# Kernel optimization log

Hardware: AMD Instinct MI355X
Metric: run time of the kernel (lower is better)

The kernel has to match this reference:

```python
import jax, jax.numpy as jnp
import numpy as np

N_NODES = 100000
N_EDGES = 1600000
DIM = 128
N_LAYERS = 3
N_GRAPHS = 128
OUT = 2


def setup_inputs() -> dict:
    key = jax.random.key(0)
    ks = jax.random.split(key, 8)
    x = jax.random.normal(ks[0], (N_NODES, DIM), dtype=jnp.float32)
    edge_index = jax.random.randint(ks[1], (2, N_EDGES), 0, N_NODES, dtype=jnp.int32)
    batch = jnp.sort(jax.random.randint(ks[2], (N_NODES,), 0, N_GRAPHS, dtype=jnp.int32))
    s = 1.0 / np.sqrt(DIM)
    conv_w = jax.random.normal(ks[3], (N_LAYERS, DIM, DIM), dtype=jnp.float32) * s
    conv_b = jnp.zeros((N_LAYERS, DIM), dtype=jnp.float32)
    lin1_w = jax.random.normal(ks[4], (DIM, DIM), dtype=jnp.float32) * s
    lin1_b = jnp.zeros((DIM,), dtype=jnp.float32)
    lin2_w = jax.random.normal(ks[5], (DIM, OUT), dtype=jnp.float32) * s
    lin2_b = jnp.zeros((OUT,), dtype=jnp.float32)
    return {"x": x, "edge_index": edge_index, "batch": batch,
            "conv_w": conv_w, "conv_b": conv_b,
            "lin1_w": lin1_w, "lin1_b": lin1_b,
            "lin2_w": lin2_w, "lin2_b": lin2_b}


def _gcn_conv(x, src, dst, norm, w, b, n_nodes):
    # linear transform first (in==out==DIM), then gather-scale-scatter
    h = x @ w                                    # [N, dim]
    msg = h[src] * norm[:, None]                 # [E+N, dim] gathered messages
    out = jax.ops.segment_sum(msg, dst, num_segments=n_nodes)
    return out + b


def reference(x, edge_index, batch, conv_w, conv_b, lin1_w, lin1_b, lin2_w, lin2_b):
    n = x.shape[0]
    loop = jnp.arange(n, dtype=edge_index.dtype)
    src = jnp.concatenate([edge_index[0], loop])  # PyG: add self-loops
    dst = jnp.concatenate([edge_index[1], loop])
    # symmetric normalization: deg computed on destination (col) with self-loops
    deg = jax.ops.segment_sum(jnp.ones_like(dst, dtype=x.dtype), dst, num_segments=n)
    deg_inv_sqrt = jnp.where(deg > 0, jax.lax.rsqrt(jnp.maximum(deg, 1.0)), 0.0)
    norm = deg_inv_sqrt[src] * deg_inv_sqrt[dst]

    h = x
    for i in range(conv_w.shape[0]):  # fixed small layer count
        h = jax.nn.relu(_gcn_conv(h, src, dst, norm, conv_w[i], conv_b[i], n))

    # global mean pool over graphs in the batch
    sums = jax.ops.segment_sum(h, batch, num_segments=N_GRAPHS)
    cnts = jax.ops.segment_sum(jnp.ones((n,), dtype=h.dtype), batch, num_segments=N_GRAPHS)
    g = sums / jnp.maximum(cnts, 1.0)[:, None]   # [G, dim]

    g = jax.nn.relu(g @ lin1_w + lin1_b)
    # dropout is inference-mode identity (training=False)
    logits = g @ lin2_w + lin2_b
    return jax.nn.log_softmax(logits, axis=-1)
```

## Files before the change

### kernel.cpp

```cpp
#include <hip/hip_runtime.h>
#include <hip/hip_fp16.h>
#include <math.h>

#define DIM 128
#define POOL_SPLIT 32
#define BINSH 10
#define EPB 8192
#define PAD 18432

typedef __attribute__((ext_vector_type(8))) _Float16 half8;
typedef __attribute__((ext_vector_type(4))) float f32x4;
typedef __attribute__((ext_vector_type(2))) float f32x2;


__global__ __launch_bounds__(1024) void bin_k(const int* __restrict__ src,
                                              const int* __restrict__ dst,
                                              int* __restrict__ bincur,
                                              unsigned int* __restrict__ tmp,
                                              int E, int NBIN) {
    __shared__ int cur[128];
    const int t = threadIdx.x;
    if (t < 128) cur[t] = 0;
    __syncthreads();
    const int e0 = blockIdx.x * EPB;
    const int e1 = min(e0 + EPB, E);
    for (int e = e0 + t; e < e1; e += 1024)
        atomicAdd(&cur[dst[e] >> BINSH], 1);
    __syncthreads();
    if (t < NBIN) {
        int h = cur[t];
        cur[t] = h ? atomicAdd(&bincur[t * 16], h) : 0;
    }
    __syncthreads();
    for (int e = e0 + t; e < e1; e += 1024) {
        int d = dst[e], s = src[e];
        int b = d >> BINSH;
        int pos = atomicAdd(&cur[b], 1);
        if (pos < PAD)
            tmp[(size_t)b * PAD + pos] =
                (unsigned int)((s << BINSH) | (d & ((1 << BINSH) - 1)));
    }
}

__global__ void binscan_k(const int* __restrict__ bincur, int* __restrict__ binbase,
                          int NBIN) {
    __shared__ int s[128];
    const int t = threadIdx.x;
    int v = (t < NBIN) ? bincur[t * 16] : 0;
    s[t] = v;
    __syncthreads();
    for (int off = 1; off < 128; off <<= 1) {
        int u = (t >= off) ? s[t - off] : 0;
        __syncthreads();
        s[t] += u;
        __syncthreads();
    }
    int excl = s[t] - v;
    if (t < NBIN) binbase[t] = excl;
    if (t == 127) binbase[NBIN] = s[127];
}

__global__ __launch_bounds__(1024) void rowcnt_k(const unsigned int* __restrict__ tmp,
                                                 const int* __restrict__ bincur,
                                                 const int* __restrict__ binbase,
                                                 int* __restrict__ rowptr,
                                                 float* __restrict__ dis,
                                                 int n, int NBIN) {
    __shared__ int cnt[1 << BINSH];
    const int b = blockIdx.x, t = threadIdx.x;
    cnt[t] = 0;
    __syncthreads();
    const int size = bincur[b * 16];
    const unsigned int* bt = tmp + (size_t)b * PAD;
    for (int e = t; e < size; e += 1024)
        atomicAdd(&cnt[bt[e] & ((1 << BINSH) - 1)], 1);
    __syncthreads();
    int v = cnt[t];
    __syncthreads();
    for (int off = 1; off < 1024; off <<= 1) {
        int u = (t >= off) ? cnt[t - off] : 0;
        __syncthreads();
        cnt[t] += u;
        __syncthreads();
    }
    int excl = cnt[t] - v;
    int node = (b << BINSH) + t;
    if (node < n) {
        rowptr[node] = binbase[b] + excl;
        dis[node] = rsqrtf((float)(v + 1));
    }
    if (b == NBIN - 1 && t == 0) rowptr[n] = binbase[NBIN];
}

__global__ __launch_bounds__(1024) void fill_k(const unsigned int* __restrict__ tmp,
                                               const int* __restrict__ bincur,
                                               const int* __restrict__ rowptr,
                                               const float* __restrict__ dis,
                                               int2* __restrict__ ew, int n) {
    __shared__ int lcur[1 << BINSH];
    __shared__ float ldis[1 << BINSH];
    const int b = blockIdx.x, t = threadIdx.x;
    const int base_node = b << BINSH;
    if (base_node + t < n) {
        lcur[t] = rowptr[base_node + t];
        ldis[t] = dis[base_node + t];
    }
    __syncthreads();
    const int size = bincur[b * 16];
    const unsigned int* bt = tmp + (size_t)b * PAD;
    for (int e = t; e < size; e += 1024) {
        unsigned int u = bt[e];
        int sidx = (int)(u >> BINSH);
        int loc = (int)(u & ((1 << BINSH) - 1));
        float w = dis[sidx] * ldis[loc];
        int q = atomicAdd(&lcur[loc], 1);
        ew[q] = make_int2(sidx, __float_as_int(w));
    }
}

__global__ void wpack_k(const float* __restrict__ conv_w, _Float16* __restrict__ bp) {
    int g = blockIdx.x * 256 + threadIdx.x;
    if (g >= 3 * 2048) return;
    int l = g >> 11;
    int rem = g & 2047;
    int c = rem >> 8;
    int f = (rem >> 6) & 3;
    int lane = rem & 63;
    const float* W = conv_w + l * DIM * DIM;
    int kbase = f * 32 + (lane >> 4) * 8;
    int col = c * 16 + (lane & 15);
    _Float16* d = bp + ((size_t)l * 2048 + (size_t)(c * 4 + f) * 64 + lane) * 8;
#pragma unroll
    for (int j = 0; j < 8; ++j)
        d[j] = (_Float16)W[(kbase + j) * DIM + col];
}

template <bool FP16IN>
__global__ __launch_bounds__(256) void gemm_k(const void* __restrict__ Ain,
                                              const _Float16* __restrict__ Bp,
                                              unsigned int* __restrict__ T32, int n) {
    const int t = threadIdx.x;
    const int lane = t & 63;
    const int wave = t >> 6;
    const int quad = lane >> 4;
    const int m    = lane & 15;
    const int row  = blockIdx.x * 64 + wave * 16 + m;
    const bool act = row < n;

    half8 a[4];
    if (act) {
        if (FP16IN) {
            const _Float16* A = (const _Float16*)Ain + (size_t)row * DIM;
#pragma unroll
            for (int f = 0; f < 4; ++f)
                a[f] = *(const half8*)(A + f * 32 + quad * 8);
        } else {
            const float* A = (const float*)Ain + (size_t)row * DIM;
#pragma unroll
            for (int f = 0; f < 4; ++f) {
                float4 v0 = *(const float4*)(A + f * 32 + quad * 8);
                float4 v1 = *(const float4*)(A + f * 32 + quad * 8 + 4);
                __half2 h01 = __floats2half2_rn(v0.x, v0.y);
                __half2 h23 = __floats2half2_rn(v0.z, v0.w);
                __half2 h45 = __floats2half2_rn(v1.x, v1.y);
                __half2 h67 = __floats2half2_rn(v1.z, v1.w);
                int4 pk;
                pk.x = *(int*)&h01; pk.y = *(int*)&h23;
                pk.z = *(int*)&h45; pk.w = *(int*)&h67;
                a[f] = *(half8*)&pk;
            }
        }
    } else {
#pragma unroll
        for (int f = 0; f < 4; ++f) a[f] = half8{};
    }

    const half8* B8 = (const half8*)Bp;
#pragma unroll
    for (int c = 0; c < 8; ++c) {
        f32x4 acc = {0.f, 0.f, 0.f, 0.f};
#pragma unroll
        for (int f = 0; f < 4; ++f) {
            half8 b = B8[(c * 4 + f) * 64 + lane];
            acc = __builtin_amdgcn_mfma_f32_16x16x32_f16(b, a[f], acc, 0, 0, 0);
        }
        if (act) {
            int r = 0;
            r = __builtin_amdgcn_cvt_pk_fp8_f32(acc[0], acc[1], r, 0);
            r = __builtin_amdgcn_cvt_pk_fp8_f32(acc[2], acc[3], r, 1);
            T32[(size_t)row * 32 + c * 4 + quad] = (unsigned int)r;
        }
    }
}

#define ACC_EDGE(qq, rr) { \
    float w = __int_as_float(qq.y); \
    f32x2 a0 = __builtin_amdgcn_cvt_pk_f32_fp8((int)rr.x, 0); \
    f32x2 a1 = __builtin_amdgcn_cvt_pk_f32_fp8((int)rr.x, 1); \
    f32x2 a2 = __builtin_amdgcn_cvt_pk_f32_fp8((int)rr.y, 0); \
    f32x2 a3 = __builtin_amdgcn_cvt_pk_f32_fp8((int)rr.y, 1); \
    acc[0] += w * a0[0]; acc[1] += w * a0[1]; \
    acc[2] += w * a1[0]; acc[3] += w * a1[1]; \
    acc[4] += w * a2[0]; acc[5] += w * a2[1]; \
    acc[6] += w * a3[0]; acc[7] += w * a3[1]; }

__global__ __launch_bounds__(256) void agg_k(const unsigned int* __restrict__ T32,
                                             const int* __restrict__ rowptr,
                                             const int2* __restrict__ ew,
                                             const float* __restrict__ dis,
                                             const float* __restrict__ bias,
                                             __half* __restrict__ O, int n) {
    const int lane = threadIdx.x & 63;
    const int qd   = lane >> 4;
    const int li   = lane & 15;
    const int v = blockIdx.x * 16 + (threadIdx.x >> 6) * 4 + qd;
    const bool act = v < n;

    const uint2* T2 = (const uint2*)T32;

    float dv = act ? dis[v] : 0.f;
    int e0 = act ? rowptr[v] : 0;
    int e1 = act ? rowptr[v + 1] : 0;

    float acc[8] = {0.f, 0.f, 0.f, 0.f, 0.f, 0.f, 0.f, 0.f};

    if (act) {
        uint2 rs = T2[(size_t)v * 16 + li];
        float w = dv * dv;
        f32x2 a0 = __builtin_amdgcn_cvt_pk_f32_fp8((int)rs.x, 0);
        f32x2 a1 = __builtin_amdgcn_cvt_pk_f32_fp8((int)rs.x, 1);
        f32x2 a2 = __builtin_amdgcn_cvt_pk_f32_fp8((int)rs.y, 0);
        f32x2 a3 = __builtin_amdgcn_cvt_pk_f32_fp8((int)rs.y, 1);
        acc[0] += w * a0[0]; acc[1] += w * a0[1];
        acc[2] += w * a1[0]; acc[3] += w * a1[1];
        acc[4] += w * a2[0]; acc[5] += w * a2[1];
        acc[6] += w * a3[0]; acc[7] += w * a3[1];
    }

    int e = e0;
    for (; e + 8 <= e1; e += 8) {
        int2 q0 = ew[e + 0], q1 = ew[e + 1], q2 = ew[e + 2], q3 = ew[e + 3];
        int2 q4 = ew[e + 4], q5 = ew[e + 5], q6 = ew[e + 6], q7 = ew[e + 7];
        uint2 r0 = T2[(size_t)q0.x * 16 + li];
        uint2 r1 = T2[(size_t)q1.x * 16 + li];
        uint2 r2 = T2[(size_t)q2.x * 16 + li];
        uint2 r3 = T2[(size_t)q3.x * 16 + li];
        uint2 r4 = T2[(size_t)q4.x * 16 + li];
        uint2 r5 = T2[(size_t)q5.x * 16 + li];
        uint2 r6 = T2[(size_t)q6.x * 16 + li];
        uint2 r7 = T2[(size_t)q7.x * 16 + li];
        ACC_EDGE(q0, r0); ACC_EDGE(q1, r1);
        ACC_EDGE(q2, r2); ACC_EDGE(q3, r3);
        ACC_EDGE(q4, r4); ACC_EDGE(q5, r5);
        ACC_EDGE(q6, r6); ACC_EDGE(q7, r7);
    }
    for (; e + 4 <= e1; e += 4) {
        int2 q0 = ew[e + 0], q1 = ew[e + 1], q2 = ew[e + 2], q3 = ew[e + 3];
        uint2 r0 = T2[(size_t)q0.x * 16 + li];
        uint2 r1 = T2[(size_t)q1.x * 16 + li];
        uint2 r2 = T2[(size_t)q2.x * 16 + li];
        uint2 r3 = T2[(size_t)q3.x * 16 + li];
        ACC_EDGE(q0, r0); ACC_EDGE(q1, r1);
        ACC_EDGE(q2, r2); ACC_EDGE(q3, r3);
    }
    for (; e + 2 <= e1; e += 2) {
        int2 q0 = ew[e + 0], q1 = ew[e + 1];
        uint2 r0 = T2[(size_t)q0.x * 16 + li];
        uint2 r1 = T2[(size_t)q1.x * 16 + li];
        ACC_EDGE(q0, r0); ACC_EDGE(q1, r1);
    }
    if (e < e1) {
        int2 q0 = ew[e];
        uint2 r0 = T2[(size_t)q0.x * 16 + li];
        ACC_EDGE(q0, r0);
    }

    if (act) {
        float4 b0 = ((const float4*)bias)[li * 2 + 0];
        float4 b1 = ((const float4*)bias)[li * 2 + 1];
        __half2 o0 = __floats2half2_rn(fmaxf(acc[0] + b0.x, 0.f), fmaxf(acc[1] + b0.y, 0.f));
        __half2 o1 = __floats2half2_rn(fmaxf(acc[2] + b0.z, 0.f), fmaxf(acc[3] + b0.w, 0.f));
        __half2 o2 = __floats2half2_rn(fmaxf(acc[4] + b1.x, 0.f), fmaxf(acc[5] + b1.y, 0.f));
        __half2 o3 = __floats2half2_rn(fmaxf(acc[6] + b1.z, 0.f), fmaxf(acc[7] + b1.w, 0.f));
        int4 o;
        o.x = *(int*)&o0; o.y = *(int*)&o1; o.z = *(int*)&o2; o.w = *(int*)&o3;
        *(int4*)(O + (size_t)v * DIM + li * 8) = o;
    }
}

__global__ __launch_bounds__(64) void pool_k(const __half* __restrict__ H,
                                             const int* __restrict__ batch,
                                             float* __restrict__ G, int n) {
    int g = blockIdx.x;
    int part = blockIdx.y;

    int lo = 0, hi = n;
    while (lo < hi) { int m = (lo + hi) >> 1; if (batch[m] < g) lo = m + 1; else hi = m; }
    int start = lo;
    lo = start; hi = n;
    while (lo < hi) { int m = (lo + hi) >> 1; if (batch[m] < g + 1) lo = m + 1; else hi = m; }
    int end = lo;
    int cnt = end - start;
    if (cnt <= 0) return;
    float inv = 1.0f / (float)cnt;

    int lane = threadIdx.x;
    const __half2* H2 = (const __half2*)H;
    float2 s = make_float2(0.f, 0.f);
    for (int v = start + part; v < end; v += POOL_SPLIT) {
        float2 h = __half22float2(H2[(size_t)v * 64 + lane]);
        s.x += h.x; s.y += h.y;
    }
    atomicAdd(&G[g * DIM + 2 * lane + 0], s.x * inv);
    atomicAdd(&G[g * DIM + 2 * lane + 1], s.y * inv);
}

__global__ __launch_bounds__(128) void head_k(const float* __restrict__ G,
                                              const float* __restrict__ l1w,
                                              const float* __restrict__ l1b,
                                              const float* __restrict__ l2w,
                                              const float* __restrict__ l2b,
                                              float* __restrict__ out) {
    int g = blockIdx.x;
    int j = threadIdx.x;
    __shared__ float gs[128];
    __shared__ float2 red[128];

    gs[j] = G[g * 128 + j];
    __syncthreads();

    float acc = l1b[j];
    for (int k = 0; k < 128; ++k) acc += gs[k] * l1w[k * 128 + j];
    float y = fmaxf(acc, 0.f);

    red[j] = make_float2(y * l2w[j * 2 + 0], y * l2w[j * 2 + 1]);
    __syncthreads();
    for (int s = 64; s > 0; s >>= 1) {
        if (j < s) {
            red[j].x += red[j + s].x;
            red[j].y += red[j + s].y;
        }
        __syncthreads();
    }
    if (j == 0) {
        float l0 = red[0].x + l2b[0];
        float l1 = red[0].y + l2b[1];
        float m = fmaxf(l0, l1);
        float lse = m + logf(expf(l0 - m) + expf(l1 - m));
        out[g * 2 + 0] = l0 - lse;
        out[g * 2 + 1] = l1 - lse;
    }
}

extern "C" void kernel_launch(void* const* d_in, const int* in_sizes, int n_in,
                              void* d_out, int out_size, void* d_ws, size_t ws_size,
                              hipStream_t stream) {
    const float* x       = (const float*)d_in[0];
    const int*   ei      = (const int*)d_in[1];
    const int*   batch   = (const int*)d_in[2];
    const float* conv_w  = (const float*)d_in[3];
    const float* conv_b  = (const float*)d_in[4];
    const float* lin1_w  = (const float*)d_in[5];
    const float* lin1_b  = (const float*)d_in[6];
    const float* lin2_w  = (const float*)d_in[7];
    const float* lin2_b  = (const float*)d_in[8];
    float* out = (float*)d_out;

    const int n = in_sizes[0] / DIM;
    const int E = in_sizes[1] / 2;
    const int n_graphs = 128;
    const int NBIN = (n + (1 << BINSH) - 1) >> BINSH;

    const int* src = ei;
    const int* dst = ei + E;

    char* p = (char*)d_ws;
    auto alloc = [&](size_t bytes) {
        char* r = p;
        p += (bytes + 255) & ~(size_t)255;
        return r;
    };
    __half*        bufH    = (__half*)alloc((size_t)n * DIM * 2);
    unsigned int*  bufT    = (unsigned int*)alloc((size_t)n * DIM);
    float*         dis     = (float*)alloc((size_t)n * 4);
    int*           rowptr  = (int*)alloc((size_t)(n + 1) * 4);
    int*           binbase = (int*)alloc(132 * 4);
    int*           bincur  = (int*)alloc((size_t)NBIN * 16 * 4);
    unsigned int*  tmp     = (unsigned int*)alloc((size_t)NBIN * PAD * 4);
    int2*          ew      = (int2*)alloc((size_t)E * 8);
    float*         gbuf    = (float*)alloc((size_t)n_graphs * DIM * 4);
    _Float16*      bp      = (_Float16*)alloc((size_t)3 * 2048 * 8 * 2);
    (void)ws_size;

    const int binBlocks = (E + EPB - 1) / EPB;

    hipMemsetAsync(bincur, 0, (size_t)NBIN * 16 * 4, stream);
    hipMemsetAsync(gbuf, 0, (size_t)n_graphs * DIM * 4, stream);
    wpack_k<<<24, 256, 0, stream>>>(conv_w, bp);
    bin_k<<<binBlocks, 1024, 0, stream>>>(src, dst, bincur, tmp, E, NBIN);
    binscan_k<<<1, 128, 0, stream>>>(bincur, binbase, NBIN);
    rowcnt_k<<<NBIN, 1024, 0, stream>>>(tmp, bincur, binbase, rowptr, dis, n, NBIN);
    fill_k<<<NBIN, 1024, 0, stream>>>(tmp, bincur, rowptr, dis, ew, n);

    const int gemmBlocks = (n + 63) / 64;
    const int aggBlocks = (n + 15) / 16;

    gemm_k<false><<<gemmBlocks, 256, 0, stream>>>((const void*)x, bp + 0 * 16384, bufT, n);
    agg_k<<<aggBlocks, 256, 0, stream>>>(bufT, rowptr, ew, dis, conv_b + 0 * DIM, bufH, n);
    gemm_k<true><<<gemmBlocks, 256, 0, stream>>>((const void*)bufH, bp + 1 * 16384, bufT, n);
    agg_k<<<aggBlocks, 256, 0, stream>>>(bufT, rowptr, ew, dis, conv_b + 1 * DIM, bufH, n);
    gemm_k<true><<<gemmBlocks, 256, 0, stream>>>((const void*)bufH, bp + 2 * 16384, bufT, n);
    agg_k<<<aggBlocks, 256, 0, stream>>>(bufT, rowptr, ew, dis, conv_b + 2 * DIM, bufH, n);

    dim3 pgrid(n_graphs, POOL_SPLIT);
    pool_k<<<pgrid, 64, 0, stream>>>(bufH, batch, gbuf, n);
    head_k<<<n_graphs, 128, 0, stream>>>(gbuf, lin1_w, lin1_b, lin2_w, lin2_b, out);
}
```

Measured before the change: 349.3 us.

## Fuse CSR build kernels, fold normalization into GEMM, merge pool and head

Merges the row-count, scan and fill kernels into one per-bin kernel that stages the bin in LDS and writes a padded CSR with per-node start/end pairs. Edges drop from (src, weight) pairs to bare indices. The source-side deg^-1/2 is now applied in the GEMM epilogue before FP8 packing, and the destination-side factor once at the end of aggregation. The memsets are folded into a prep kernel, and pool plus head become a single kernel with 128 blocks. This cuts launches and edge-list bandwidth, but pooling now runs on far fewer threads, and scaling before FP8 quantization changes rounding behaviour.

```diff
diff --git a/kernel.cpp b/kernel.cpp
--- a/kernel.cpp
+++ b/kernel.cpp
@@ -3,7 +3,6 @@
 #include <math.h>
 
 #define DIM 128
-#define POOL_SPLIT 32
 #define BINSH 10
 #define EPB 8192
 #define PAD 18432
@@ -12,114 +11,11 @@
 typedef __attribute__((ext_vector_type(4))) float f32x4;
 typedef __attribute__((ext_vector_type(2))) float f32x2;
 
-
-__global__ __launch_bounds__(1024) void bin_k(const int* __restrict__ src,
-                                              const int* __restrict__ dst,
-                                              int* __restrict__ bincur,
-                                              unsigned int* __restrict__ tmp,
-                                              int E, int NBIN) {
-    __shared__ int cur[128];
-    const int t = threadIdx.x;
-    if (t < 128) cur[t] = 0;
-    __syncthreads();
-    const int e0 = blockIdx.x * EPB;
-    const int e1 = min(e0 + EPB, E);
-    for (int e = e0 + t; e < e1; e += 1024)
-        atomicAdd(&cur[dst[e] >> BINSH], 1);
-    __syncthreads();
-    if (t < NBIN) {
-        int h = cur[t];
-        cur[t] = h ? atomicAdd(&bincur[t * 16], h) : 0;
-    }
-    __syncthreads();
-    for (int e = e0 + t; e < e1; e += 1024) {
-        int d = dst[e], s = src[e];
-        int b = d >> BINSH;
-        int pos = atomicAdd(&cur[b], 1);
-        if (pos < PAD)
-            tmp[(size_t)b * PAD + pos] =
-                (unsigned int)((s << BINSH) | (d & ((1 << BINSH) - 1)));
-    }
-}
-
-__global__ void binscan_k(const int* __restrict__ bincur, int* __restrict__ binbase,
-                          int NBIN) {
-    __shared__ int s[128];
-    const int t = threadIdx.x;
-    int v = (t < NBIN) ? bincur[t * 16] : 0;
-    s[t] = v;
-    __syncthreads();
-    for (int off = 1; off < 128; off <<= 1) {
-        int u = (t >= off) ? s[t - off] : 0;
-        __syncthreads();
-        s[t] += u;
-        __syncthreads();
-    }
-    int excl = s[t] - v;
-    if (t < NBIN) binbase[t] = excl;
-    if (t == 127) binbase[NBIN] = s[127];
-}
-
-__global__ __launch_bounds__(1024) void rowcnt_k(const unsigned int* __restrict__ tmp,
-                                                 const int* __restrict__ bincur,
-                                                 const int* __restrict__ binbase,
-                                                 int* __restrict__ rowptr,
-                                                 float* __restrict__ dis,
-                                                 int n, int NBIN) {
-    __shared__ int cnt[1 << BINSH];
-    const int b = blockIdx.x, t = threadIdx.x;
-    cnt[t] = 0;
-    __syncthreads();
-    const int size = bincur[b * 16];
-    const unsigned int* bt = tmp + (size_t)b * PAD;
-    for (int e = t; e < size; e += 1024)
-        atomicAdd(&cnt[bt[e] & ((1 << BINSH) - 1)], 1);
-    __syncthreads();
-    int v = cnt[t];
-    __syncthreads();
-    for (int off = 1; off < 1024; off <<= 1) {
-        int u = (t >= off) ? cnt[t - off] : 0;
-        __syncthreads();
-        cnt[t] += u;
-        __syncthreads();
-    }
-    int excl = cnt[t] - v;
-    int node = (b << BINSH) + t;
-    if (node < n) {
-        rowptr[node] = binbase[b] + excl;
-        dis[node] = rsqrtf((float)(v + 1));
-    }
-    if (b == NBIN - 1 && t == 0) rowptr[n] = binbase[NBIN];
-}
-
-__global__ __launch_bounds__(1024) void fill_k(const unsigned int* __restrict__ tmp,
-                                               const int* __restrict__ bincur,
-                                               const int* __restrict__ rowptr,
-                                               const float* __restrict__ dis,
-                                               int2* __restrict__ ew, int n) {
-    __shared__ int lcur[1 << BINSH];
-    __shared__ float ldis[1 << BINSH];
-    const int b = blockIdx.x, t = threadIdx.x;
-    const int base_node = b << BINSH;
-    if (base_node + t < n) {
-        lcur[t] = rowptr[base_node + t];
-        ldis[t] = dis[base_node + t];
-    }
-    __syncthreads();
-    const int size = bincur[b * 16];
-    const unsigned int* bt = tmp + (size_t)b * PAD;
-    for (int e = t; e < size; e += 1024) {
-        unsigned int u = bt[e];
-        int sidx = (int)(u >> BINSH);
-        int loc = (int)(u & ((1 << BINSH) - 1));
-        float w = dis[sidx] * ldis[loc];
-        int q = atomicAdd(&lcur[loc], 1);
-        ew[q] = make_int2(sidx, __float_as_int(w));
-    }
-}
-
-__global__ void wpack_k(const float* __restrict__ conv_w, _Float16* __restrict__ bp) {
+__global__ __launch_bounds__(256) void prep_k(const float* __restrict__ conv_w,
+                                              _Float16* __restrict__ bp,
+                                              int* __restrict__ bincur, int nbc) {
     int g = blockIdx.x * 256 + threadIdx.x;
+    if (g < nbc) bincur[g] = 0;
     if (g >= 3 * 2048) return;
     int l = g >> 11;
     int rem = g & 2047;
@@ -135,9 +31,79 @@
         d[j] = (_Float16)W[(kbase + j) * DIM + col];
 }
 
+__global__ __launch_bounds__(1024) void bin_k(const int* __restrict__ src,
+                                              const int* __restrict__ dst,
+                                              int* __restrict__ bincur,
+                                              unsigned int* __restrict__ tmp,
+                                              int E, int NBIN) {
+    __shared__ int cur[128];
+    const int t = threadIdx.x;
+    if (t < 128) cur[t] = 0;
+    __syncthreads();
+    const int e0 = blockIdx.x * EPB;
+    const int e1 = min(e0 + EPB, E);
+    for (int e = e0 + t; e < e1; e += 1024)
+        atomicAdd(&cur[dst[e] >> BINSH], 1);
+    __syncthreads();
+    if (t < NBIN) {
+        int h = cur[t];
+        cur[t] = h ? atomicAdd(&bincur[t * 16], h) : 0;
+    }
+    __syncthreads();
+    for (int e = e0 + t; e < e1; e += 1024) {
+        int d = dst[e], s = src[e];
+        int b = d >> BINSH;
+        int pos = atomicAdd(&cur[b], 1);
+        if (pos < PAD)
+            tmp[(size_t)b * PAD + pos] =
+                (unsigned int)((s << BINSH) | (d & ((1 << BINSH) - 1)));
+    }
+}
+
+__global__ __launch_bounds__(1024) void fused_k(const unsigned int* __restrict__ tmp,
+                                                const int* __restrict__ bincur,
+                                                int2* __restrict__ rowse,
+                                                float* __restrict__ dis,
+                                                int* __restrict__ ew, int n) {
+    __shared__ unsigned int led[PAD];
+    __shared__ int cnt[1 << BINSH];
+    __shared__ int lcur[1 << BINSH];
+    const int b = blockIdx.x, t = threadIdx.x;
+    const int size = min(bincur[b * 16], PAD);
+    const unsigned int* bt = tmp + (size_t)b * PAD;
+    cnt[t] = 0;
+    for (int e = t; e < size; e += 1024) led[e] = bt[e];
+    __syncthreads();
+    for (int e = t; e < size; e += 1024)
+        atomicAdd(&cnt[led[e] & ((1 << BINSH) - 1)], 1);
+    __syncthreads();
+    int v = cnt[t];
+    __syncthreads();
+    for (int off = 1; off < 1024; off <<= 1) {
+        int u = (t >= off) ? cnt[t - off] : 0;
+        __syncthreads();
+        cnt[t] += u;
+        __syncthreads();
+    }
+    int start = b * PAD + cnt[t] - v;
+    lcur[t] = start;
+    int node = (b << BINSH) + t;
+    if (node < n) {
+        rowse[node] = make_int2(start, start + v);
+        dis[node] = rsqrtf((float)(v + 1));
+    }
+    __syncthreads();
+    for (int e = t; e < size; e += 1024) {
+        unsigned int u = led[e];
+        int q = atomicAdd(&lcur[u & ((1 << BINSH) - 1)], 1);
+        ew[q] = (int)(u >> BINSH);
+    }
+}
+
 template <bool FP16IN>
 __global__ __launch_bounds__(256) void gemm_k(const void* __restrict__ Ain,
                                               const _Float16* __restrict__ Bp,
+                                              const float* __restrict__ dis,
                                               unsigned int* __restrict__ T32, int n) {
     const int t = threadIdx.x;
     const int lane = t & 63;
@@ -148,7 +114,9 @@
     const bool act = row < n;
 
     half8 a[4];
+    float dvr = 0.f;
     if (act) {
+        dvr = dis[row];
         if (FP16IN) {
             const _Float16* A = (const _Float16*)Ain + (size_t)row * DIM;
 #pragma unroll
@@ -186,113 +154,112 @@
         }
         if (act) {
             int r = 0;
-            r = __builtin_amdgcn_cvt_pk_fp8_f32(acc[0], acc[1], r, 0);
-            r = __builtin_amdgcn_cvt_pk_fp8_f32(acc[2], acc[3], r, 1);
+            r = __builtin_amdgcn_cvt_pk_fp8_f32(dvr * acc[0], dvr * acc[1], r, 0);
+            r = __builtin_amdgcn_cvt_pk_fp8_f32(dvr * acc[2], dvr * acc[3], r, 1);
             T32[(size_t)row * 32 + c * 4 + quad] = (unsigned int)r;
         }
     }
 }
 
-#define ACC_EDGE(qq, rr) { \
-    float w = __int_as_float(qq.y); \
+#define ACC_EDGE(rr) { \
     f32x2 a0 = __builtin_amdgcn_cvt_pk_f32_fp8((int)rr.x, 0); \
     f32x2 a1 = __builtin_amdgcn_cvt_pk_f32_fp8((int)rr.x, 1); \
     f32x2 a2 = __builtin_amdgcn_cvt_pk_f32_fp8((int)rr.y, 0); \
     f32x2 a3 = __builtin_amdgcn_cvt_pk_f32_fp8((int)rr.y, 1); \
-    acc[0] += w * a0[0]; acc[1] += w * a0[1]; \
-    acc[2] += w * a1[0]; acc[3] += w * a1[1]; \
-    acc[4] += w * a2[0]; acc[5] += w * a2[1]; \
-    acc[6] += w * a3[0]; acc[7] += w * a3[1]; }
+    acc[0] += a0[0]; acc[1] += a0[1]; \
+    acc[2] += a1[0]; acc[3] += a1[1]; \
+    acc[4] += a2[0]; acc[5] += a2[1]; \
+    acc[6] += a3[0]; acc[7] += a3[1]; }
 
 __global__ __launch_bounds__(256) void agg_k(const unsigned int* __restrict__ T32,
-                                             const int* __restrict__ rowptr,
-                                             const int2* __restrict__ ew,
+                                             const int2* __restrict__ rowse,
+                                             const int* __restrict__ ew,
                                              const float* __restrict__ dis,
                                              const float* __restrict__ bias,
                                              __half* __restrict__ O, int n) {
     const int lane = threadIdx.x & 63;
-    const int qd   = lane >> 4;
     const int li   = lane & 15;
-    const int v = blockIdx.x * 16 + (threadIdx.x >> 6) * 4 + qd;
+    const int v = blockIdx.x * 16 + (threadIdx.x >> 6) * 4 + (lane >> 4);
     const bool act = v < n;
 
     const uint2* T2 = (const uint2*)T32;
 
-    float dv = act ? dis[v] : 0.f;
-    int e0 = act ? rowptr[v] : 0;
-    int e1 = act ? rowptr[v + 1] : 0;
+    int e0 = 0, e1 = 0;
+    float dv = 0.f;
+    if (act) {
+        int2 re = rowse[v];
+        e0 = re.x; e1 = re.y;
+        dv = dis[v];
+    }
 
     float acc[8] = {0.f, 0.f, 0.f, 0.f, 0.f, 0.f, 0.f, 0.f};
 
     if (act) {
         uint2 rs = T2[(size_t)v * 16 + li];
-        float w = dv * dv;
-        f32x2 a0 = __builtin_amdgcn_cvt_pk_f32_fp8((int)rs.x, 0);
-        f32x2 a1 = __builtin_amdgcn_cvt_pk_f32_fp8((int)rs.x, 1);
-        f32x2 a2 = __builtin_amdgcn_cvt_pk_f32_fp8((int)rs.y, 0);
-        f32x2 a3 = __builtin_amdgcn_cvt_pk_f32_fp8((int)rs.y, 1);
-        acc[0] += w * a0[0]; acc[1] += w * a0[1];
-        acc[2] += w * a1[0]; acc[3] += w * a1[1];
-        acc[4] += w * a2[0]; acc[5] += w * a2[1];
-        acc[6] += w * a3[0]; acc[7] += w * a3[1];
+        ACC_EDGE(rs);
     }
 
     int e = e0;
     for (; e + 8 <= e1; e += 8) {
-        int2 q0 = ew[e + 0], q1 = ew[e + 1], q2 = ew[e + 2], q3 = ew[e + 3];
-        int2 q4 = ew[e + 4], q5 = ew[e + 5], q6 = ew[e + 6], q7 = ew[e + 7];
-        uint2 r0 = T2[(size_t)q0.x * 16 + li];
-        uint2 r1 = T2[(size_t)q1.x * 16 + li];
-        uint2 r2 = T2[(size_t)q2.x * 16 + li];
-        uint2 r3 = T2[(size_t)q3.x * 16 + li];
-        uint2 r4 = T2[(size_t)q4.x * 16 + li];
-        uint2 r5 = T2[(size_t)q5.x * 16 + li];
-        uint2 r6 = T2[(size_t)q6.x * 16 + li];
-        uint2 r7 = T2[(size_t)q7.x * 16 + li];
-        ACC_EDGE(q0, r0); ACC_EDGE(q1, r1);
-        ACC_EDGE(q2, r2); ACC_EDGE(q3, r3);
-        ACC_EDGE(q4, r4); ACC_EDGE(q5, r5);
-        ACC_EDGE(q6, r6); ACC_EDGE(q7, r7);
+        int c0 = ew[e + 0], c1 = ew[e + 1], c2 = ew[e + 2], c3 = ew[e + 3];
+        int c4 = ew[e + 4], c5 = ew[e + 5], c6 = ew[e + 6], c7 = ew[e + 7];
+        uint2 r0 = T2[(size_t)c0 * 16 + li];
+        uint2 r1 = T2[(size_t)c1 * 16 + li];
+        uint2 r2 = T2[(size_t)c2 * 16 + li];
+        uint2 r3 = T2[(size_t)c3 * 16 + li];
+        uint2 r4 = T2[(size_t)c4 * 16 + li];
+        uint2 r5 = T2[(size_t)c5 * 16 + li];
+        uint2 r6 = T2[(size_t)c6 * 16 + li];
+        uint2 r7 = T2[(size_t)c7 * 16 + li];
+        ACC_EDGE(r0); ACC_EDGE(r1); ACC_EDGE(r2); ACC_EDGE(r3);
+        ACC_EDGE(r4); ACC_EDGE(r5); ACC_EDGE(r6); ACC_EDGE(r7);
     }
     for (; e + 4 <= e1; e += 4) {
-        int2 q0 = ew[e + 0], q1 = ew[e + 1], q2 = ew[e + 2], q3 = ew[e + 3];
-        uint2 r0 = T2[(size_t)q0.x * 16 + li];
-        uint2 r1 = T2[(size_t)q1.x * 16 + li];
-        uint2 r2 = T2[(size_t)q2.x * 16 + li];
-        uint2 r3 = T2[(size_t)q3.x * 16 + li];
-        ACC_EDGE(q0, r0); ACC_EDGE(q1, r1);
-        ACC_EDGE(q2, r2); ACC_EDGE(q3, r3);
+        int c0 = ew[e + 0], c1 = ew[e + 1], c2 = ew[e + 2], c3 = ew[e + 3];
+        uint2 r0 = T2[(size_t)c0 * 16 + li];
+        uint2 r1 = T2[(size_t)c1 * 16 + li];
+        uint2 r2 = T2[(size_t)c2 * 16 + li];
+        uint2 r3 = T2[(size_t)c3 * 16 + li];
+        ACC_EDGE(r0); ACC_EDGE(r1); ACC_EDGE(r2); ACC_EDGE(r3);
     }
     for (; e + 2 <= e1; e += 2) {
-        int2 q0 = ew[e + 0], q1 = ew[e + 1];
-        uint2 r0 = T2[(size_t)q0.x * 16 + li];
-        uint2 r1 = T2[(size_t)q1.x * 16 + li];
-        ACC_EDGE(q0, r0); ACC_EDGE(q1, r1);
+        int c0 = ew[e + 0], c1 = ew[e + 1];
+        uint2 r0 = T2[(size_t)c0 * 16 + li];
+        uint2 r1 = T2[(size_t)c1 * 16 + li];
+        ACC_EDGE(r0); ACC_EDGE(r1);
     }
     if (e < e1) {
-        int2 q0 = ew[e];
-        uint2 r0 = T2[(size_t)q0.x * 16 + li];
-        ACC_EDGE(q0, r0);
+        uint2 r0 = T2[(size_t)ew[e] * 16 + li];
+        ACC_EDGE(r0);
     }
 
     if (act) {
         float4 b0 = ((const float4*)bias)[li * 2 + 0];
         float4 b1 = ((const float4*)bias)[li * 2 + 1];
-        __half2 o0 = __floats2half2_rn(fmaxf(acc[0] + b0.x, 0.f), fmaxf(acc[1] + b0.y, 0.f));
-        __half2 o1 = __floats2half2_rn(fmaxf(acc[2] + b0.z, 0.f), fmaxf(acc[3] + b0.w, 0.f));
-        __half2 o2 = __floats2half2_rn(fmaxf(acc[4] + b1.x, 0.f), fmaxf(acc[5] + b1.y, 0.f));
-        __half2 o3 = __floats2half2_rn(fmaxf(acc[6] + b1.z, 0.f), fmaxf(acc[7] + b1.w, 0.f));
+        __half2 o0 = __floats2half2_rn(fmaxf(dv * acc[0] + b0.x, 0.f),
+                                       fmaxf(dv * acc[1] + b0.y, 0.f));
+        __half2 o1 = __floats2half2_rn(fmaxf(dv * acc[2] + b0.z, 0.f),
+                                       fmaxf(dv * acc[3] + b0.w, 0.f));
+        __half2 o2 = __floats2half2_rn(fmaxf(dv * acc[4] + b1.x, 0.f),
+                                       fmaxf(dv * acc[5] + b1.y, 0.f));
+        __half2 o3 = __floats2half2_rn(fmaxf(dv * acc[6] + b1.z, 0.f),
+                                       fmaxf(dv * acc[7] + b1.w, 0.f));
         int4 o;
         o.x = *(int*)&o0; o.y = *(int*)&o1; o.z = *(int*)&o2; o.w = *(int*)&o3;
         *(int4*)(O + (size_t)v * DIM + li * 8) = o;
     }
 }
 
-__global__ __launch_bounds__(64) void pool_k(const __half* __restrict__ H,
-                                             const int* __restrict__ batch,
-                                             float* __restrict__ G, int n) {
-    int g = blockIdx.x;
-    int part = blockIdx.y;
+__global__ __launch_bounds__(128) void poolhead_k(const __half* __restrict__ H,
+                                                  const int* __restrict__ batch,
+                                                  const float* __restrict__ l1w,
+                                                  const float* __restrict__ l1b,
+                                                  const float* __restrict__ l2w,
+                                                  const float* __restrict__ l2b,
+                                                  float* __restrict__ out, int n) {
+    const int g = blockIdx.x, j = threadIdx.x;
+    __shared__ float gs[128];
+    __shared__ float2 red[128];
 
     int lo = 0, hi = n;
     while (lo < hi) { int m = (lo + hi) >> 1; if (batch[m] < g) lo = m + 1; else hi = m; }
@@ -301,32 +268,22 @@
     while (lo < hi) { int m = (lo + hi) >> 1; if (batch[m] < g + 1) lo = m + 1; else hi = m; }
     int end = lo;
     int cnt = end - start;
-    if (cnt <= 0) return;
-    float inv = 1.0f / (float)cnt;
-
-    int lane = threadIdx.x;
+
     const __half2* H2 = (const __half2*)H;
+    const int half = j >> 6, lane = j & 63;
     float2 s = make_float2(0.f, 0.f);
-    for (int v = start + part; v < end; v += POOL_SPLIT) {
+    for (int v = start + half; v < end; v += 2) {
         float2 h = __half22float2(H2[(size_t)v * 64 + lane]);
         s.x += h.x; s.y += h.y;
     }
-    atomicAdd(&G[g * DIM + 2 * lane + 0], s.x * inv);
-    atomicAdd(&G[g * DIM + 2 * lane + 1], s.y * inv);
-}
-
-__global__ __launch_bounds__(128) void head_k(const float* __restrict__ G,
-                                              const float* __restrict__ l1w,
-                                              const float* __restrict__ l1b,
-                                              const float* __restrict__ l2w,
-                                              const float* __restrict__ l2b,
-                                              float* __restrict__ out) {
-    int g = blockIdx.x;
-    int j = threadIdx.x;
-    __shared__ float gs[128];
-    __shared__ float2 red[128];
-
-    gs[j] = G[g * 128 + j];
+    red[j] = s;
+    __syncthreads();
+    if (j < 64) {
+        float inv = cnt > 0 ? 1.f / (float)cnt : 0.f;
+        float2 a = red[j], b = red[j + 64];
+        gs[2 * j + 0] = (a.x + b.x) * inv;
+        gs[2 * j + 1] = (a.y + b.y) * inv;
+    }
     __syncthreads();
 
     float acc = l1b[j];
@@ -335,10 +292,10 @@
 
     red[j] = make_float2(y * l2w[j * 2 + 0], y * l2w[j * 2 + 1]);
     __syncthreads();
-    for (int s = 64; s > 0; s >>= 1) {
-        if (j < s) {
-            red[j].x += red[j + s].x;
-            red[j].y += red[j + s].y;
+    for (int sfd = 64; sfd > 0; sfd >>= 1) {
+        if (j < sfd) {
+            red[j].x += red[j + sfd].x;
+            red[j].y += red[j + sfd].y;
         }
         __syncthreads();
     }
@@ -383,36 +340,28 @@
     __half*        bufH    = (__half*)alloc((size_t)n * DIM * 2);
     unsigned int*  bufT    = (unsigned int*)alloc((size_t)n * DIM);
     float*         dis     = (float*)alloc((size_t)n * 4);
-    int*           rowptr  = (int*)alloc((size_t)(n + 1) * 4);
-    int*           binbase = (int*)alloc(132 * 4);
+    int2*          rowse   = (int2*)alloc((size_t)n * 8);
     int*           bincur  = (int*)alloc((size_t)NBIN * 16 * 4);
     unsigned int*  tmp     = (unsigned int*)alloc((size_t)NBIN * PAD * 4);
-    int2*          ew      = (int2*)alloc((size_t)E * 8);
-    float*         gbuf    = (float*)alloc((size_t)n_graphs * DIM * 4);
+    int*           ew      = (int*)alloc((size_t)NBIN * PAD * 4);
     _Float16*      bp      = (_Float16*)alloc((size_t)3 * 2048 * 8 * 2);
     (void)ws_size;
 
     const int binBlocks = (E + EPB - 1) / EPB;
 
-    hipMemsetAsync(bincur, 0, (size_t)NBIN * 16 * 4, stream);
-    hipMemsetAsync(gbuf, 0, (size_t)n_graphs * DIM * 4, stream);
-    wpack_k<<<24, 256, 0, stream>>>(conv_w, bp);
+    prep_k<<<24, 256, 0, stream>>>(conv_w, bp, bincur, NBIN * 16);
     bin_k<<<binBlocks, 1024, 0, stream>>>(src, dst, bincur, tmp, E, NBIN);
-    binscan_k<<<1, 128, 0, stream>>>(bincur, binbase, NBIN);
-    rowcnt_k<<<NBIN, 1024, 0, stream>>>(tmp, bincur, binbase, rowptr, dis, n, NBIN);
-    fill_k<<<NBIN, 1024, 0, stream>>>(tmp, bincur, rowptr, dis, ew, n);
+    fused_k<<<NBIN, 1024, 0, stream>>>(tmp, bincur, rowse, dis, ew, n);
 
     const int gemmBlocks = (n + 63) / 64;
     const int aggBlocks = (n + 15) / 16;
 
-    gemm_k<false><<<gemmBlocks, 256, 0, stream>>>((const void*)x, bp + 0 * 16384, bufT, n);
-    agg_k<<<aggBlocks, 256, 0, stream>>>(bufT, rowptr, ew, dis, conv_b + 0 * DIM, bufH, n);
-    gemm_k<true><<<gemmBlocks, 256, 0, stream>>>((const void*)bufH, bp + 1 * 16384, bufT, n);
-    agg_k<<<aggBlocks, 256, 0, stream>>>(bufT, rowptr, ew, dis, conv_b + 1 * DIM, bufH, n);
-    gemm_k<true><<<gemmBlocks, 256, 0, stream>>>((const void*)bufH, bp + 2 * 16384, bufT, n);
-    agg_k<<<aggBlocks, 256, 0, stream>>>(bufT, rowptr, ew, dis, conv_b + 2 * DIM, bufH, n);
-
-    dim3 pgrid(n_graphs, POOL_SPLIT);
-    pool_k<<<pgrid, 64, 0, stream>>>(bufH, batch, gbuf, n);
-    head_k<<<n_graphs, 128, 0, stream>>>(gbuf, lin1_w, lin1_b, lin2_w, lin2_b, out);
-}
+    gemm_k<false><<<gemmBlocks, 256, 0, stream>>>((const void*)x, bp + 0 * 16384, dis, bufT, n);
+    agg_k<<<aggBlocks, 256, 0, stream>>>(bufT, rowse, ew, dis, conv_b + 0 * DIM, bufH, n);
+    gemm_k<true><<<gemmBlocks, 256, 0, stream>>>((const void*)bufH, bp + 1 * 16384, dis, bufT, n);
+    agg_k<<<aggBlocks, 256, 0, stream>>>(bufT, rowse, ew, dis, conv_b + 1 * DIM, bufH, n);
+    gemm_k<true><<<gemmBlocks, 256, 0, stream>>>((const void*)bufH, bp + 2 * 16384, dis, bufT, n);
+    agg_k<<<aggBlocks, 256, 0, stream>>>(bufT, rowse, ew, dis, conv_b + 2 * DIM, bufH, n);
+
+    poolhead_k<<<n_graphs, 128, 0, stream>>>(bufH, batch, lin1_w, lin1_b, lin2_w, lin2_b, out, n);
+}
```

After: 410.9 us. 1.18x slower.
